# Kernel tuning notes

Measured on AMD Instinct MI355X. Metric: run time of the kernel, lower is better.

The kernel has to match this reference:

```python
import jax, jax.numpy as jnp
import numpy as np

B, C, H, W = 8, 128, 64, 64
U, TOP_K, L, HID = 8, 2, 10, 128


def setup_inputs() -> dict:
    key = jax.random.key(0)
    ks = jax.random.split(key, 16)
    rn = lambda k, shp, s=0.05: jax.random.normal(k, shp, jnp.float32) * s
    return {
        "x": jax.random.normal(ks[0], (B, C, H, W), jnp.float32),
        # router shared MLP (torch Linear: y = x @ W.T + b)
        "W1": rn(ks[1], (HID, C)), "b1": rn(ks[2], (HID,), 0.01),
        "W2": rn(ks[3], (HID, HID)), "b2": rn(ks[4], (HID,), 0.01),
        "W3": rn(ks[5], (HID // 2, HID)), "b3": rn(ks[6], (HID // 2,), 0.01),
        "W4": rn(ks[7], (HID // 2, HID // 2)), "b4": rn(ks[8], (HID // 2,), 0.01),
        "Wu": rn(ks[9], (U, HID // 2)), "bu": rn(ks[10], (U,), 0.01),
        "Wc": rn(ks[11], (L, HID // 2)), "bc": rn(ks[12], (L,), 0.01),
        # per-unit 3x3 convs stacked for a grouped conv: [U*Cout, Cin, 3, 3]
        "conv_w": rn(ks[13], (U * C, C, 3, 3), 0.05),
        "conv_b": rn(ks[14], (U * C,), 0.01),
    }


def reference(x, W1, b1, W2, b2, W3, b3, W4, b4, Wu, bu, Wc, bc, conv_w, conv_b):
    Bt, Ct, Ht, Wt = x.shape
    # --- TopKRouter ---
    pooled = x.mean(axis=(2, 3))                      # adaptive avg pool to 1x1 -> [B,C]
    h = jax.nn.relu(pooled @ W1.T + b1)
    h = jax.nn.relu(h @ W2.T + b2)
    h = jax.nn.relu(h @ W3.T + b3)
    feat = h @ W4.T + b4                              # [B, 64]
    unit_scores = feat @ Wu.T + bu                    # [B, U]
    cls_logits = feat @ Wc.T + bc                     # [B, L]
    noise = jax.random.normal(jax.random.key(42), unit_scores.shape, unit_scores.dtype) * 0.01
    unit_scores = unit_scores + noise
    top_v, top_i = jax.lax.top_k(unit_scores, TOP_K)  # [B, K]
    probabilities = jax.nn.softmax(top_v, axis=1)     # computed in original (unused in combine)
    del probabilities
    unit_usage = jnp.zeros((U,), x.dtype).at[top_i.reshape(-1)].add(1.0) / (Bt * TOP_K)
    lb_loss = ((unit_usage - unit_usage.mean()) ** 2).mean()
    l2_reg = 0.01 * sum(jnp.linalg.norm(p) for p in
                        [W1, b1, W2, b2, W3, b3, W4, b4, Wu, bu, Wc, bc])
    # --- scatter-dispatch: unit u gets x if u in top-k indices else zeros ---
    mask = (top_i[:, :, None] == jnp.arange(U)[None, None, :]).any(axis=1)  # [B, U]
    unit_in = x[:, None] * mask[:, :, None, None, None].astype(x.dtype)     # [B,U,C,H,W]
    # --- per-unit conv as one grouped conv ---
    lhs = unit_in.reshape(Bt, U * Ct, Ht, Wt)
    out = jax.lax.conv_general_dilated(
        lhs, conv_w, window_strides=(1, 1), padding="SAME",
        dimension_numbers=("NCHW", "OIHW", "NCHW"), feature_group_count=U)
    out = out + conv_b[None, :, None, None]
    combined = out.reshape(Bt, U, -1, Ht, Wt)          # [B,U,Cout,H,W]
    # --- gated combine ---
    gate = jax.nn.softmax(combined.mean(axis=(2, 3, 4)), axis=-1)  # [B, U]
    final = jnp.einsum("buchw,bu->bchw", combined, gate)
    return (final, cls_logits, l2_reg, top_i, lb_loss)
```

## Files before the change

### kernel.cpp

```cpp
#include <hip/hip_runtime.h>
#include <math.h>

#define Bn   8
#define Cn   128
#define Hn   64
#define Wn   64
#define HWn  4096
#define Un   8
#define Ln   10
#define HIDn 128

#define OUT_FINAL 0
#define OUT_CLS   4194304
#define OUT_L2    4194384
#define OUT_TOPI  4194385
#define OUT_LB    4194401

#define WS_POOLED 0
#define WS_STR    1024
#define WS_TOPI   10240
#define WS_GSEL   10256
#define WS_BIASC  10272
#define WS_L2P    11296
#define WS_GSUM   11308
#define WS_BSUM   11372
#define WS_H1     11380
#define WS_H2     12404
#define WS_H3     13428
#define WS_FEAT   13940
#define WS_W9P    14452
#define WS_XT     88180
#define WS_WCOMB  2185332

#define NOISE_PARTITIONABLE 1

typedef __attribute__((ext_vector_type(8))) short bf16x8;
typedef __attribute__((ext_vector_type(4))) float f32x4;

__device__ __forceinline__ unsigned short f2bf(float f) {
    unsigned u = __float_as_uint(f);
    unsigned r = (u + 0x7fffu + ((u >> 16) & 1u)) >> 16;
    return (unsigned short)r;
}

__device__ __forceinline__ unsigned rotl32(unsigned x, int d) {
    return (x << d) | (x >> (32 - d));
}

__device__ __forceinline__ void threefry2x32(unsigned k1, unsigned k2,
                                             unsigned c0, unsigned c1,
                                             unsigned* o0, unsigned* o1) {
    unsigned ks0 = k1, ks1 = k2, ks2 = k1 ^ k2 ^ 0x1BD11BDAu;
    unsigned ksa[3] = {ks0, ks1, ks2};
    const int rot[2][4] = {{13, 15, 26, 6}, {17, 29, 16, 24}};
    unsigned x0 = c0 + ks0, x1 = c1 + ks1;
    #pragma unroll
    for (int s = 0; s < 5; ++s) {
        #pragma unroll
        for (int q = 0; q < 4; ++q) {
            x0 += x1;
            x1 = rotl32(x1, rot[s & 1][q]);
            x1 ^= x0;
        }
        x0 += ksa[(s + 1) % 3];
        x1 += ksa[(s + 2) % 3] + (unsigned)(s + 1);
    }
    *o0 = x0;
    *o1 = x1;
}

__device__ float jax_noise_elem(int i) {
    unsigned o0, o1, bits;
#if NOISE_PARTITIONABLE
    threefry2x32(0u, 42u, 0u, (unsigned)i, &o0, &o1);
    bits = o0 ^ o1;
#else
    {
        int second = (i >= 32);
        unsigned j = (unsigned)(second ? i - 32 : i);
        threefry2x32(0u, 42u, j, j + 32u, &o0, &o1);
        bits = second ? o1 : o0;
    }
#endif
    unsigned fb = (bits >> 9) | 0x3f800000u;
    float f = __uint_as_float(fb) - 1.0f;
    const float lo = __uint_as_float(0xBF7FFFFFu);
    float u = f * (1.0f - lo) + lo;
    u = fmaxf(lo, u);
    float w = -log1pf(-u * u);
    float p;
    if (w < 5.0f) {
        w = w - 2.5f;
        p = 2.81022636e-08f;
        p = fmaf(p, w, 3.43273939e-07f);
        p = fmaf(p, w, -3.5233877e-06f);
        p = fmaf(p, w, -4.39150654e-06f);
        p = fmaf(p, w, 0.00021858087f);
        p = fmaf(p, w, -0.00125372503f);
        p = fmaf(p, w, -0.00417768164f);
        p = fmaf(p, w, 0.246640727f);
        p = fmaf(p, w, 1.50140941f);
    } else {
        w = sqrtf(w) - 3.0f;
        p = -0.000200214257f;
        p = fmaf(p, w, 0.000100950558f);
        p = fmaf(p, w, 0.00134934322f);
        p = fmaf(p, w, -0.00367342844f);
        p = fmaf(p, w, 0.00573950773f);
        p = fmaf(p, w, -0.0076224613f);
        p = fmaf(p, w, 0.00943887047f);
        p = fmaf(p, w, 1.00167406f);
        p = fmaf(p, w, 2.83297682f);
    }
    float n = 1.41421356237309515f * (p * u);
    return n * 0.01f;
}

__global__ __launch_bounds__(256) void prep_kernel(
    const float* __restrict__ x, const float* __restrict__ cw,
    const float* __restrict__ W1, const float* __restrict__ b1,
    const float* __restrict__ W2, const float* __restrict__ b2,
    const float* __restrict__ W3, const float* __restrict__ b3,
    const float* __restrict__ W4, const float* __restrict__ b4,
    const float* __restrict__ Wu, const float* __restrict__ bu,
    const float* __restrict__ Wc, const float* __restrict__ bc,
    float* __restrict__ ws) {
    __shared__ float smem[8256];
    int bid = blockIdx.x;
    int tid = threadIdx.x;

    if (bid < 512) {
        int b = bid >> 6, y = bid & 63;
        #pragma unroll
        for (int k = 0; k < 32; ++k) {
            int cin = (tid >> 6) + (k << 2);
            int xcol = tid & 63;
            smem[xcol * 129 + cin] =
                x[(((size_t)b * 128 + cin) << 12) + (y << 6) + xcol];
        }
        __syncthreads();
        unsigned short* xtp = (unsigned short*)(ws + WS_XT);
        #pragma unroll
        for (int i = 0; i < 4; ++i) {
            int op = tid + (i << 8);
            int px = op >> 4, part = op & 15;
            const float* src = smem + px * 129 + part * 8;
            uint4 u;
            u.x = (unsigned)f2bf(src[0]) | ((unsigned)f2bf(src[1]) << 16);
            u.y = (unsigned)f2bf(src[2]) | ((unsigned)f2bf(src[3]) << 16);
            u.z = (unsigned)f2bf(src[4]) | ((unsigned)f2bf(src[5]) << 16);
            u.w = (unsigned)f2bf(src[6]) | ((unsigned)f2bf(src[7]) << 16);
            *(uint4*)(xtp + (((((size_t)b * 64 + y) * 64 + px) << 7) + (part << 3))) = u;
        }
    } else if (bid < 1536) {
        int bc_ = bid - 512;
        const float4* p4 = (const float4*)(x + (size_t)bc_ * HWn);
        float vals[5] = {0.f, 0.f, 0.f, 0.f, 0.f};
        #pragma unroll
        for (int it = 0; it < 4; ++it) {
            int i = tid + it * 256;
            float4 v = p4[i];
            float s4 = v.x + v.y + v.z + v.w;
            vals[0] += s4;
            if (i < 16) vals[1] += s4;
            if (i >= 1008) vals[2] += s4;
            if ((i & 15) == 0) vals[3] += v.x;
            if ((i & 15) == 15) vals[4] += v.w;
            if (i == 0) ws[WS_STR + bc_ * 9 + 5] = v.x;
            if (i == 15) ws[WS_STR + bc_ * 9 + 6] = v.w;
            if (i == 1008) ws[WS_STR + bc_ * 9 + 7] = v.x;
            if (i == 1023) ws[WS_STR + bc_ * 9 + 8] = v.w;
        }
        #pragma unroll
        for (int q = 0; q < 5; ++q)
            #pragma unroll
            for (int off = 32; off > 0; off >>= 1)
                vals[q] += __shfl_xor(vals[q], off);
        int wave = tid >> 6, lane = tid & 63;
        if (lane == 0) {
            #pragma unroll
            for (int q = 0; q < 5; ++q) smem[wave * 5 + q] = vals[q];
        }
        __syncthreads();
        if (tid < 5) {
            float o = smem[tid] + smem[5 + tid] + smem[10 + tid] + smem[15 + tid];
            ws[WS_STR + bc_ * 9 + tid] = o;
            if (tid == 0) ws[WS_POOLED + bc_] = o * (1.0f / HWn);
        }
    } else if (bid < 1600) {
        int idx = bid - 1536;
        int u = idx >> 3, g = idx & 7;
        const float* base = cw + (size_t)u * 147456 + (size_t)g * 18432;
        float a0 = 0.f, a1 = 0.f, a2 = 0.f, a3 = 0.f, a4 = 0.f;
        #pragma unroll
        for (int cout = 0; cout < 16; ++cout) {
            const float* row = base + (size_t)cout * 1152;
            a0 += row[tid];
            a1 += row[tid + 256];
            a2 += row[tid + 512];
            a3 += row[tid + 768];
            if (tid < 128) a4 += row[tid + 1024];
        }
        float* dst = ws + WS_W9P + (size_t)idx * 1152;
        dst[tid] = a0;
        dst[tid + 256] = a1;
        dst[tid + 512] = a2;
        dst[tid + 768] = a3;
        if (tid < 128) dst[tid + 1024] = a4;
    } else {
        int idx = bid - 1600;
        const float* ptab[12] = {W1, b1, W2, b2, W3, b3, W4, b4, Wu, bu, Wc, bc};
        const int ntab[12] = {16384, 128, 16384, 128, 8192, 64, 4096, 64, 512, 8, 640, 10};
        const float* p = ptab[idx];
        int n = ntab[idx];
        float s = 0.f;
        for (int i = tid; i < n; i += 256) { float v = p[i]; s = fmaf(v, v, s); }
        #pragma unroll
        for (int off = 32; off > 0; off >>= 1) s += __shfl_xor(s, off);
        int wave = tid >> 6, lane = tid & 63;
        if (lane == 0) smem[wave] = s;
        __syncthreads();
        if (tid == 0) ws[WS_L2P + idx] = smem[0] + smem[1] + smem[2] + smem[3];
    }
}

__global__ __launch_bounds__(256) void gsum_kernel(const float* __restrict__ cb,
                                                   float* __restrict__ ws) {
    int bid = blockIdx.x;
    int b = bid >> 3, u = bid & 7;
    int tid = threadIdx.x;
    __shared__ float T[1152];
    __shared__ float red[4];

    if (tid < 128) {
        const float* st = ws + WS_STR + (b * 128 + tid) * 9;
        float S = st[0], R0 = st[1], R63 = st[2], C0 = st[3], C63 = st[4];
        float c00 = st[5], c0r = st[6], cb0 = st[7], cbr = st[8];
        float Rex[3] = {R63, 0.f, R0};
        float Cex[3] = {C63, 0.f, C0};
        float crn[3][3] = {{cbr, 0.f, cb0}, {0.f, 0.f, 0.f}, {c0r, 0.f, c00}};
        #pragma unroll
        for (int ky = 0; ky < 3; ++ky)
            #pragma unroll
            for (int kx = 0; kx < 3; ++kx)
                T[tid * 9 + ky * 3 + kx] = S - Rex[ky] - Cex[kx] + crn[ky][kx];
    }
    __syncthreads();

    float s = 0.f;
    #pragma unroll
    for (int g = 0; g < 8; ++g) {
        const float* row = ws + WS_W9P + (size_t)((u << 3) + g) * 1152;
        #pragma unroll
        for (int i = 0; i < 4; ++i)
            s = fmaf(row[tid + i * 256], T[tid + i * 256], s);
        if (tid < 128) s = fmaf(row[tid + 1024], T[tid + 1024], s);
    }
    #pragma unroll
    for (int off = 32; off > 0; off >>= 1) s += __shfl_xor(s, off);
    int wave = tid >> 6, lane = tid & 63;
    if (lane == 0) red[wave] = s;
    __syncthreads();
    if (tid == 0) ws[WS_GSUM + bid] = red[0] + red[1] + red[2] + red[3];

    if (b == 0) {
        float t2 = (tid < 128) ? cb[u * 128 + tid] : 0.f;
        #pragma unroll
        for (int off = 32; off > 0; off >>= 1) t2 += __shfl_xor(t2, off);
        if (lane == 0) red[wave] = t2;
        __syncthreads();
        if (tid == 0) ws[WS_BSUM + u] = red[0] + red[1] + red[2] + red[3];
    }
}

__global__ __launch_bounds__(256) void mlp128_kernel(
    const float* __restrict__ W, const float* __restrict__ bias,
    const float* __restrict__ inp, float* __restrict__ outp,
    int outStride, int doRelu) {
    __shared__ float in_s[1024];
    int tid = threadIdx.x;
    for (int i = tid; i < 1024; i += 256) in_s[i] = inp[i];
    __syncthreads();
    int r = tid >> 5, l = tid & 31;
    int j = blockIdx.x * 8 + r;
    float4 w = ((const float4*)(W + j * 128))[l];
    float bj = bias[j];
    #pragma unroll
    for (int b = 0; b < 8; ++b) {
        const float* sp = in_s + b * 128 + l * 4;
        float s = w.x * sp[0] + w.y * sp[1] + w.z * sp[2] + w.w * sp[3];
        s += __shfl_xor(s, 16, 32); s += __shfl_xor(s, 8, 32);
        s += __shfl_xor(s, 4, 32);  s += __shfl_xor(s, 2, 32);
        s += __shfl_xor(s, 1, 32);
        if (l == 0) {
            s += bj;
            outp[b * outStride + j] = doRelu ? fmaxf(s, 0.f) : s;
        }
    }
}

__global__ __launch_bounds__(256) void mlp64_kernel(
    const float* __restrict__ W, const float* __restrict__ bias,
    const float* __restrict__ inp, float* __restrict__ outp) {
    __shared__ float in_s[512];
    int tid = threadIdx.x;
    for (int i = tid; i < 512; i += 256) in_s[i] = inp[i];
    __syncthreads();
    int r = tid >> 5, l = tid & 31;
    int j = blockIdx.x * 8 + r;
    float2 w = ((const float2*)(W + j * 64))[l];
    float bj = bias[j];
    #pragma unroll
    for (int b = 0; b < 8; ++b) {
        const float* sp = in_s + b * 64 + l * 2;
        float s = w.x * sp[0] + w.y * sp[1];
        s += __shfl_xor(s, 16, 32); s += __shfl_xor(s, 8, 32);
        s += __shfl_xor(s, 4, 32);  s += __shfl_xor(s, 2, 32);
        s += __shfl_xor(s, 1, 32);
        if (l == 0) outp[b * 64 + j] = s + bj;
    }
}

__global__ __launch_bounds__(256) void score_gate_kernel(
    const float* __restrict__ Wu, const float* __restrict__ bu,
    const float* __restrict__ Wc, const float* __restrict__ bc,
    const float* __restrict__ cb,
    float* __restrict__ ws, float* __restrict__ out) {
    __shared__ float feat[512];
    __shared__ float scores[64];
    __shared__ float noise[64];
    __shared__ int topi[16];
    __shared__ float gate_sh[64];
    int tid = threadIdx.x;
    int grp = tid >> 4, l = tid & 15;

    for (int i = tid; i < 512; i += 256) feat[i] = ws[WS_FEAT + i];
    __syncthreads();

    if (tid < 64) noise[tid] = jax_noise_elem(tid);
    if (grp < 8) {
        int j = grp;
        float4 wa = ((const float4*)(Wu + j * 64))[l];
        float bj = bu[j];
        #pragma unroll
        for (int b = 0; b < 8; ++b) {
            const float* sp = feat + b * 64 + l * 4;
            float s = wa.x * sp[0] + wa.y * sp[1] + wa.z * sp[2] + wa.w * sp[3];
            s += __shfl_xor(s, 8, 16); s += __shfl_xor(s, 4, 16);
            s += __shfl_xor(s, 2, 16); s += __shfl_xor(s, 1, 16);
            if (l == 0) scores[b * 8 + j] = s + bj;
        }
    }
    if (grp < 10) {
        int j = grp;
        float4 wa = ((const float4*)(Wc + j * 64))[l];
        float bj = bc[j];
        #pragma unroll
        for (int b = 0; b < 8; ++b) {
            const float* sp = feat + b * 64 + l * 4;
            float s = wa.x * sp[0] + wa.y * sp[1] + wa.z * sp[2] + wa.w * sp[3];
            s += __shfl_xor(s, 8, 16); s += __shfl_xor(s, 4, 16);
            s += __shfl_xor(s, 2, 16); s += __shfl_xor(s, 1, 16);
            if (l == 0) out[OUT_CLS + b * 10 + j] = s + bj;
        }
    }
    __syncthreads();
    if (tid < 64) scores[tid] += noise[tid];
    __syncthreads();
    if (tid < Bn) {
        int b = tid;
        float best = -1e30f; int bi = 0;
        for (int u = 0; u < Un; ++u) {
            float v = scores[b * Un + u];
            if (v > best) { best = v; bi = u; }
        }
        float best2 = -1e30f; int bi2 = 0;
        for (int u = 0; u < Un; ++u) {
            if (u == bi) continue;
            float v = scores[b * Un + u];
            if (v > best2) { best2 = v; bi2 = u; }
        }
        topi[b * 2] = bi;
        topi[b * 2 + 1] = bi2;
        ((int*)ws)[WS_TOPI + b * 2] = bi;
        ((int*)ws)[WS_TOPI + b * 2 + 1] = bi2;
        out[OUT_TOPI + b * 2] = (float)bi;
        out[OUT_TOPI + b * 2 + 1] = (float)bi2;
    }
    __syncthreads();
    if (tid == 0) {
        int cnt[Un];
        for (int u = 0; u < Un; ++u) cnt[u] = 0;
        for (int i = 0; i < Bn * 2; ++i) cnt[topi[i]]++;
        float lb = 0.f;
        for (int u = 0; u < Un; ++u) {
            float d = (float)cnt[u] * (1.f / 16.f) - 0.125f;
            lb += d * d;
        }
        out[OUT_LB] = lb * (1.f / Un);
        float l2 = 0.f;
        #pragma unroll
        for (int i = 0; i < 12; ++i) l2 += sqrtf(ws[WS_L2P + i]);
        out[OUT_L2] = 0.01f * l2;
    }
    if (tid < Bn) {
        int b2 = tid;
        int s0 = topi[b2 * 2], s1 = topi[b2 * 2 + 1];
        float lg[Un];
        for (int u2 = 0; u2 < Un; ++u2) lg[u2] = ws[WS_BSUM + u2] * (1.0f / Cn);
        lg[s0] += ws[WS_GSUM + b2 * 8 + s0] * (1.0f / (Cn * HWn));
        lg[s1] += ws[WS_GSUM + b2 * 8 + s1] * (1.0f / (Cn * HWn));
        float m = -1e30f;
        for (int u2 = 0; u2 < Un; ++u2) m = fmaxf(m, lg[u2]);
        float den = 0.f, e[Un];
        for (int u2 = 0; u2 < Un; ++u2) { e[u2] = expf(lg[u2] - m); den += e[u2]; }
        float inv = 1.0f / den;
        for (int u2 = 0; u2 < Un; ++u2) gate_sh[b2 * Un + u2] = e[u2] * inv;
        ws[WS_GSEL + b2 * 2] = gate_sh[b2 * Un + s0];
        ws[WS_GSEL + b2 * 2 + 1] = gate_sh[b2 * Un + s1];
    }
    __syncthreads();
    for (int i = tid; i < Bn * Cn; i += 256) {
        int b2 = i >> 7, c = i & 127;
        float s = 0.f;
        for (int u2 = 0; u2 < Un; ++u2)
            s = fmaf(gate_sh[b2 * Un + u2], cb[u2 * Cn + c], s);
        ws[WS_BIASC + i] = s;
    }
}

__global__ __launch_bounds__(256) void wprep_kernel(const float* __restrict__ cw,
                                                    float* __restrict__ ws) {
    int bid = blockIdx.x;
    int b = bid >> 5, g = bid & 31;
    const int* topi = (const int*)ws + WS_TOPI;
    int u0 = topi[b * 2], u1 = topi[b * 2 + 1];
    float g0 = ws[WS_GSEL + b * 2], g1 = ws[WS_GSEL + b * 2 + 1];
    __shared__ float lds[1152];
    unsigned short* wc = (unsigned short*)(ws + WS_WCOMB);
    int tid = threadIdx.x;
    for (int co = 0; co < 4; ++co) {
        int cout = g * 4 + co;
        const float* r0 = cw + ((size_t)u0 * 128 + cout) * 1152;
        const float* r1 = cw + ((size_t)u1 * 128 + cout) * 1152;
        if (co) __syncthreads();
        #pragma unroll
        for (int i = 0; i < 5; ++i) {
            int e = tid + i * 256;
            if (e < 1152) lds[e] = g0 * r0[e] + g1 * r1[e];
        }
        __syncthreads();
        #pragma unroll
        for (int i = 0; i < 3; ++i) {
            int p = tid + i * 256;
            if (p < 576) {
                int tap = p >> 6, cp = p & 63;
                unsigned lo = f2bf(lds[(2 * cp) * 9 + tap]);
                unsigned hi = f2bf(lds[(2 * cp + 1) * 9 + tap]);
                *(unsigned*)(wc + ((((size_t)(b * 128 + cout) * 9 + tap) << 7)
                                   + 2 * cp)) = lo | (hi << 16);
            }
        }
    }
}

__global__ __launch_bounds__(128) void conv_mfma_kernel(
    const float* __restrict__ wsf, float* __restrict__ out) {
    const unsigned short* __restrict__ xt = (const unsigned short*)(wsf + WS_XT);
    const unsigned short* __restrict__ wc = (const unsigned short*)(wsf + WS_WCOMB);

    int bid = blockIdx.x;
    int b = bid >> 6, y = bid & 63;
    int tid = threadIdx.x;
    int wave = tid >> 6, lane = tid & 63;
    int quad = lane >> 4, l15 = lane & 15;
    int m0 = wave << 6;

    __shared__ __align__(16) unsigned short xs[198 * 136];

    f32x4 acc[4][4];
    #pragma unroll
    for (int mt = 0; mt < 4; ++mt)
        #pragma unroll
        for (int nt = 0; nt < 4; ++nt)
            acc[mt][nt] = (f32x4){0.f, 0.f, 0.f, 0.f};

    #pragma unroll
    for (int i = 0; i < 25; ++i) {
        int o = tid + i * 128;
        if (o < 3168) {
            int px = o >> 4, part = o & 15;
            int r3 = (unsigned)px / 66u;
            int col = px - r3 * 66;
            int ry = y + r3 - 1;
            int gx = col - 1;
            uint4 v = {0u, 0u, 0u, 0u};
            if ((unsigned)ry < 64u && (unsigned)gx < 64u) {
                v = *(const uint4*)(xt +
                    ((((size_t)b * 64 + ry) * 64 + gx) << 7) + (part << 3));
            }
            *(uint4*)((char*)xs + px * 272 + part * 16) = v;
        }
    }
    __syncthreads();

    int ldsrd = l15 * 272 + quad * 16;
    #pragma unroll
    for (int tap = 0; tap < 9; ++tap) {
        const int dy = tap / 3, dx = tap % 3;
        #pragma unroll
        for (int chunk = 0; chunk < 4; ++chunk) {
            bf16x8 af[4];
            #pragma unroll
            for (int mt = 0; mt < 4; ++mt) {
                int cout = m0 + mt * 16 + l15;
                af[mt] = *(const bf16x8*)(wc +
                    (((size_t)(b * 128 + cout) * 9 + tap) << 7) +
                    (chunk << 5) + (quad << 3));
            }
            bf16x8 bfr[4];
            #pragma unroll
            for (int nt = 0; nt < 4; ++nt) {
                int off = (dy * 66 + dx + nt * 16) * 272 + (chunk << 6);
                bfr[nt] = *(const bf16x8*)((char*)xs + ldsrd + off);
            }
            #pragma unroll
            for (int mt = 0; mt < 4; ++mt)
                #pragma unroll
                for (int nt = 0; nt < 4; ++nt)
                    acc[mt][nt] = __builtin_amdgcn_mfma_f32_16x16x32_bf16(
                        af[mt], bfr[nt], acc[mt][nt], 0, 0, 0);
        }
    }

    #pragma unroll
    for (int mt = 0; mt < 4; ++mt) {
        #pragma unroll
        for (int r = 0; r < 4; ++r) {
            int c = m0 + mt * 16 + (quad << 2) + r;
            float bias = wsf[WS_BIASC + (b << 7) + c];
            size_t rowb = (((size_t)b * 128 + c) << 12) + (y << 6);
            #pragma unroll
            for (int nt = 0; nt < 4; ++nt)
                out[rowb + nt * 16 + l15] = acc[mt][nt][r] + bias;
        }
    }
}

extern "C" void kernel_launch(void* const* d_in, const int* in_sizes, int n_in,
                              void* d_out, int out_size, void* d_ws, size_t ws_size,
                              hipStream_t stream) {
    const float* x  = (const float*)d_in[0];
    const float* W1 = (const float*)d_in[1];
    const float* b1 = (const float*)d_in[2];
    const float* W2 = (const float*)d_in[3];
    const float* b2 = (const float*)d_in[4];
    const float* W3 = (const float*)d_in[5];
    const float* b3 = (const float*)d_in[6];
    const float* W4 = (const float*)d_in[7];
    const float* b4 = (const float*)d_in[8];
    const float* Wu = (const float*)d_in[9];
    const float* bu = (const float*)d_in[10];
    const float* Wc = (const float*)d_in[11];
    const float* bc = (const float*)d_in[12];
    const float* cw = (const float*)d_in[13];
    const float* cb = (const float*)d_in[14];
    float* out = (float*)d_out;
    float* ws  = (float*)d_ws;

    prep_kernel<<<1612, 256, 0, stream>>>(x, cw, W1, b1, W2, b2, W3, b3,
                                          W4, b4, Wu, bu, Wc, bc, ws);
    gsum_kernel<<<64, 256, 0, stream>>>(cb, ws);
    mlp128_kernel<<<16, 256, 0, stream>>>(W1, b1, ws + WS_POOLED, ws + WS_H1, 128, 1);
    mlp128_kernel<<<16, 256, 0, stream>>>(W2, b2, ws + WS_H1, ws + WS_H2, 128, 1);
    mlp128_kernel<<<8, 256, 0, stream>>>(W3, b3, ws + WS_H2, ws + WS_H3, 64, 1);
    mlp64_kernel<<<8, 256, 0, stream>>>(W4, b4, ws + WS_H3, ws + WS_FEAT);
    score_gate_kernel<<<1, 256, 0, stream>>>(Wu, bu, Wc, bc, cb, ws, out);
    wprep_kernel<<<256, 256, 0, stream>>>(cw, ws);
    conv_mfma_kernel<<<512, 128, 0, stream>>>(ws, out);
}
```

Measured before the change: 189.2 us.

## Fuse router MLP, gsum and gating kernels into one grid-barrier kernel

Replaces six small sequential launches (gsum, four MLP layers, score/gate) with one persistent 80-block kernel that uses atomic grid barriers between stages. The gsum work runs alongside the first MLP layer, and the bias-combine step is spread across four blocks. This removes several kernel-launch and drain gaps on the critical path. In exchange it relies on all 80 blocks being co-resident and on a barrier counter that prep_kernel resets, and it adds spin-wait cost at each barrier.

New measurement: 203.9 us. 7.8% more time.

```diff
diff --git a/kernel.cpp b/kernel.cpp
--- a/kernel.cpp
+++ b/kernel.cpp
@@ -28,11 +28,14 @@
 #define WS_H2     12404
 #define WS_H3     13428
 #define WS_FEAT   13940
-#define WS_W9P    14452
-#define WS_XT     88180
-#define WS_WCOMB  2185332
+#define WS_GATE   14452
+#define WS_BAR    14516
+#define WS_W9P    14524
+#define WS_XT     88252
+#define WS_WCOMB  2185404
 
 #define NOISE_PARTITIONABLE 1
+#define RGRID 80u
 
 typedef __attribute__((ext_vector_type(8))) short bf16x8;
 typedef __attribute__((ext_vector_type(4))) float f32x4;
@@ -41,6 +44,17 @@
     unsigned u = __float_as_uint(f);
     unsigned r = (u + 0x7fffu + ((u >> 16) & 1u)) >> 16;
     return (unsigned short)r;
+}
+
+__device__ __forceinline__ void grid_bar(unsigned* bar, int slot) {
+    __syncthreads();
+    if (threadIdx.x == 0) {
+        unsigned* c = bar + slot;
+        __hip_atomic_fetch_add(c, 1u, __ATOMIC_ACQ_REL, __HIP_MEMORY_SCOPE_AGENT);
+        while (__hip_atomic_load(c, __ATOMIC_ACQUIRE, __HIP_MEMORY_SCOPE_AGENT) < RGRID)
+            __builtin_amdgcn_s_sleep(1);
+    }
+    __syncthreads();
 }
 
 __device__ __forceinline__ unsigned rotl32(unsigned x, int d) {
@@ -190,6 +204,7 @@
     } else if (bid < 1600) {
         int idx = bid - 1536;
         int u = idx >> 3, g = idx & 7;
+        if (idx == 0 && tid < 8) ((unsigned*)(ws + WS_BAR))[tid] = 0u;
         const float* base = cw + (size_t)u * 147456 + (size_t)g * 18432;
         float a0 = 0.f, a1 = 0.f, a2 = 0.f, a3 = 0.f, a4 = 0.f;
         #pragma unroll
@@ -224,207 +239,242 @@
     }
 }
 
-__global__ __launch_bounds__(256) void gsum_kernel(const float* __restrict__ cb,
-                                                   float* __restrict__ ws) {
-    int bid = blockIdx.x;
-    int b = bid >> 3, u = bid & 7;
-    int tid = threadIdx.x;
-    __shared__ float T[1152];
-    __shared__ float red[4];
-
-    if (tid < 128) {
-        const float* st = ws + WS_STR + (b * 128 + tid) * 9;
-        float S = st[0], R0 = st[1], R63 = st[2], C0 = st[3], C63 = st[4];
-        float c00 = st[5], c0r = st[6], cb0 = st[7], cbr = st[8];
-        float Rex[3] = {R63, 0.f, R0};
-        float Cex[3] = {C63, 0.f, C0};
-        float crn[3][3] = {{cbr, 0.f, cb0}, {0.f, 0.f, 0.f}, {c0r, 0.f, c00}};
-        #pragma unroll
-        for (int ky = 0; ky < 3; ++ky)
-            #pragma unroll
-            for (int kx = 0; kx < 3; ++kx)
-                T[tid * 9 + ky * 3 + kx] = S - Rex[ky] - Cex[kx] + crn[ky][kx];
-    }
-    __syncthreads();
-
-    float s = 0.f;
-    #pragma unroll
-    for (int g = 0; g < 8; ++g) {
-        const float* row = ws + WS_W9P + (size_t)((u << 3) + g) * 1152;
-        #pragma unroll
-        for (int i = 0; i < 4; ++i)
-            s = fmaf(row[tid + i * 256], T[tid + i * 256], s);
-        if (tid < 128) s = fmaf(row[tid + 1024], T[tid + 1024], s);
-    }
-    #pragma unroll
-    for (int off = 32; off > 0; off >>= 1) s += __shfl_xor(s, off);
-    int wave = tid >> 6, lane = tid & 63;
-    if (lane == 0) red[wave] = s;
-    __syncthreads();
-    if (tid == 0) ws[WS_GSUM + bid] = red[0] + red[1] + red[2] + red[3];
-
-    if (b == 0) {
-        float t2 = (tid < 128) ? cb[u * 128 + tid] : 0.f;
-        #pragma unroll
-        for (int off = 32; off > 0; off >>= 1) t2 += __shfl_xor(t2, off);
-        if (lane == 0) red[wave] = t2;
-        __syncthreads();
-        if (tid == 0) ws[WS_BSUM + u] = red[0] + red[1] + red[2] + red[3];
-    }
-}
-
-__global__ __launch_bounds__(256) void mlp128_kernel(
-    const float* __restrict__ W, const float* __restrict__ bias,
-    const float* __restrict__ inp, float* __restrict__ outp,
-    int outStride, int doRelu) {
-    __shared__ float in_s[1024];
-    int tid = threadIdx.x;
-    for (int i = tid; i < 1024; i += 256) in_s[i] = inp[i];
-    __syncthreads();
-    int r = tid >> 5, l = tid & 31;
-    int j = blockIdx.x * 8 + r;
-    float4 w = ((const float4*)(W + j * 128))[l];
-    float bj = bias[j];
-    #pragma unroll
-    for (int b = 0; b < 8; ++b) {
-        const float* sp = in_s + b * 128 + l * 4;
-        float s = w.x * sp[0] + w.y * sp[1] + w.z * sp[2] + w.w * sp[3];
-        s += __shfl_xor(s, 16, 32); s += __shfl_xor(s, 8, 32);
-        s += __shfl_xor(s, 4, 32);  s += __shfl_xor(s, 2, 32);
-        s += __shfl_xor(s, 1, 32);
-        if (l == 0) {
-            s += bj;
-            outp[b * outStride + j] = doRelu ? fmaxf(s, 0.f) : s;
-        }
-    }
-}
-
-__global__ __launch_bounds__(256) void mlp64_kernel(
-    const float* __restrict__ W, const float* __restrict__ bias,
-    const float* __restrict__ inp, float* __restrict__ outp) {
-    __shared__ float in_s[512];
-    int tid = threadIdx.x;
-    for (int i = tid; i < 512; i += 256) in_s[i] = inp[i];
-    __syncthreads();
-    int r = tid >> 5, l = tid & 31;
-    int j = blockIdx.x * 8 + r;
-    float2 w = ((const float2*)(W + j * 64))[l];
-    float bj = bias[j];
-    #pragma unroll
-    for (int b = 0; b < 8; ++b) {
-        const float* sp = in_s + b * 64 + l * 2;
-        float s = w.x * sp[0] + w.y * sp[1];
-        s += __shfl_xor(s, 16, 32); s += __shfl_xor(s, 8, 32);
-        s += __shfl_xor(s, 4, 32);  s += __shfl_xor(s, 2, 32);
-        s += __shfl_xor(s, 1, 32);
-        if (l == 0) outp[b * 64 + j] = s + bj;
-    }
-}
-
-__global__ __launch_bounds__(256) void score_gate_kernel(
+__global__ __launch_bounds__(256) void router_fused_kernel(
+    const float* __restrict__ W1, const float* __restrict__ b1,
+    const float* __restrict__ W2, const float* __restrict__ b2,
+    const float* __restrict__ W3, const float* __restrict__ b3,
+    const float* __restrict__ W4, const float* __restrict__ b4,
     const float* __restrict__ Wu, const float* __restrict__ bu,
     const float* __restrict__ Wc, const float* __restrict__ bc,
     const float* __restrict__ cb,
     float* __restrict__ ws, float* __restrict__ out) {
-    __shared__ float feat[512];
-    __shared__ float scores[64];
-    __shared__ float noise[64];
-    __shared__ int topi[16];
-    __shared__ float gate_sh[64];
+    __shared__ float sh[1216];
+    int bid = blockIdx.x;
     int tid = threadIdx.x;
-    int grp = tid >> 4, l = tid & 15;
-
-    for (int i = tid; i < 512; i += 256) feat[i] = ws[WS_FEAT + i];
-    __syncthreads();
-
-    if (tid < 64) noise[tid] = jax_noise_elem(tid);
-    if (grp < 8) {
-        int j = grp;
-        float4 wa = ((const float4*)(Wu + j * 64))[l];
-        float bj = bu[j];
+    unsigned* bar = (unsigned*)(ws + WS_BAR);
+
+    if (bid < 16) {
+        for (int i = tid; i < 1024; i += 256) sh[i] = ws[WS_POOLED + i];
+        __syncthreads();
+        int r = tid >> 5, l = tid & 31;
+        int j = bid * 8 + r;
+        float4 w = ((const float4*)(W1 + j * 128))[l];
+        float bj = b1[j];
         #pragma unroll
         for (int b = 0; b < 8; ++b) {
-            const float* sp = feat + b * 64 + l * 4;
-            float s = wa.x * sp[0] + wa.y * sp[1] + wa.z * sp[2] + wa.w * sp[3];
-            s += __shfl_xor(s, 8, 16); s += __shfl_xor(s, 4, 16);
-            s += __shfl_xor(s, 2, 16); s += __shfl_xor(s, 1, 16);
-            if (l == 0) scores[b * 8 + j] = s + bj;
-        }
-    }
-    if (grp < 10) {
-        int j = grp;
-        float4 wa = ((const float4*)(Wc + j * 64))[l];
-        float bj = bc[j];
+            const float* sp = sh + b * 128 + l * 4;
+            float s = w.x * sp[0] + w.y * sp[1] + w.z * sp[2] + w.w * sp[3];
+            s += __shfl_xor(s, 16, 32); s += __shfl_xor(s, 8, 32);
+            s += __shfl_xor(s, 4, 32);  s += __shfl_xor(s, 2, 32);
+            s += __shfl_xor(s, 1, 32);
+            if (l == 0) ws[WS_H1 + b * 128 + j] = fmaxf(s + bj, 0.f);
+        }
+    } else {
+        int idx = bid - 16;
+        int b = idx >> 3, u = idx & 7;
+        float* T = sh;
+        float* red = sh + 1152;
+        if (tid < 128) {
+            const float* st = ws + WS_STR + (b * 128 + tid) * 9;
+            float S = st[0], R0 = st[1], R63 = st[2], C0 = st[3], C63 = st[4];
+            float c00 = st[5], c0r = st[6], cb0 = st[7], cbr = st[8];
+            float Rex[3] = {R63, 0.f, R0};
+            float Cex[3] = {C63, 0.f, C0};
+            float crn[3][3] = {{cbr, 0.f, cb0}, {0.f, 0.f, 0.f}, {c0r, 0.f, c00}};
+            #pragma unroll
+            for (int ky = 0; ky < 3; ++ky)
+                #pragma unroll
+                for (int kx = 0; kx < 3; ++kx)
+                    T[tid * 9 + ky * 3 + kx] = S - Rex[ky] - Cex[kx] + crn[ky][kx];
+        }
+        __syncthreads();
+        float s = 0.f;
+        #pragma unroll
+        for (int g = 0; g < 8; ++g) {
+            const float* row = ws + WS_W9P + (size_t)((u << 3) + g) * 1152;
+            #pragma unroll
+            for (int i = 0; i < 4; ++i)
+                s = fmaf(row[tid + i * 256], T[tid + i * 256], s);
+            if (tid < 128) s = fmaf(row[tid + 1024], T[tid + 1024], s);
+        }
+        #pragma unroll
+        for (int off = 32; off > 0; off >>= 1) s += __shfl_xor(s, off);
+        int wave = tid >> 6, lane = tid & 63;
+        if (lane == 0) red[wave] = s;
+        __syncthreads();
+        if (tid == 0) ws[WS_GSUM + idx] = red[0] + red[1] + red[2] + red[3];
+        if (b == 0) {
+            float t2 = (tid < 128) ? cb[u * 128 + tid] : 0.f;
+            #pragma unroll
+            for (int off = 32; off > 0; off >>= 1) t2 += __shfl_xor(t2, off);
+            if (lane == 0) red[wave] = t2;
+            __syncthreads();
+            if (tid == 0) ws[WS_BSUM + u] = red[0] + red[1] + red[2] + red[3];
+        }
+    }
+    grid_bar(bar, 0);
+
+    if (bid < 16) {
+        for (int i = tid; i < 1024; i += 256) sh[i] = ws[WS_H1 + i];
+        __syncthreads();
+        int r = tid >> 5, l = tid & 31;
+        int j = bid * 8 + r;
+        float4 w = ((const float4*)(W2 + j * 128))[l];
+        float bj = b2[j];
         #pragma unroll
         for (int b = 0; b < 8; ++b) {
-            const float* sp = feat + b * 64 + l * 4;
-            float s = wa.x * sp[0] + wa.y * sp[1] + wa.z * sp[2] + wa.w * sp[3];
-            s += __shfl_xor(s, 8, 16); s += __shfl_xor(s, 4, 16);
-            s += __shfl_xor(s, 2, 16); s += __shfl_xor(s, 1, 16);
-            if (l == 0) out[OUT_CLS + b * 10 + j] = s + bj;
-        }
-    }
-    __syncthreads();
-    if (tid < 64) scores[tid] += noise[tid];
-    __syncthreads();
-    if (tid < Bn) {
-        int b = tid;
-        float best = -1e30f; int bi = 0;
-        for (int u = 0; u < Un; ++u) {
-            float v = scores[b * Un + u];
-            if (v > best) { best = v; bi = u; }
-        }
-        float best2 = -1e30f; int bi2 = 0;
-        for (int u = 0; u < Un; ++u) {
-            if (u == bi) continue;
-            float v = scores[b * Un + u];
-            if (v > best2) { best2 = v; bi2 = u; }
-        }
-        topi[b * 2] = bi;
-        topi[b * 2 + 1] = bi2;
-        ((int*)ws)[WS_TOPI + b * 2] = bi;
-        ((int*)ws)[WS_TOPI + b * 2 + 1] = bi2;
-        out[OUT_TOPI + b * 2] = (float)bi;
-        out[OUT_TOPI + b * 2 + 1] = (float)bi2;
-    }
-    __syncthreads();
-    if (tid == 0) {
-        int cnt[Un];
-        for (int u = 0; u < Un; ++u) cnt[u] = 0;
-        for (int i = 0; i < Bn * 2; ++i) cnt[topi[i]]++;
-        float lb = 0.f;
-        for (int u = 0; u < Un; ++u) {
-            float d = (float)cnt[u] * (1.f / 16.f) - 0.125f;
-            lb += d * d;
-        }
-        out[OUT_LB] = lb * (1.f / Un);
-        float l2 = 0.f;
-        #pragma unroll
-        for (int i = 0; i < 12; ++i) l2 += sqrtf(ws[WS_L2P + i]);
-        out[OUT_L2] = 0.01f * l2;
-    }
-    if (tid < Bn) {
-        int b2 = tid;
-        int s0 = topi[b2 * 2], s1 = topi[b2 * 2 + 1];
-        float lg[Un];
-        for (int u2 = 0; u2 < Un; ++u2) lg[u2] = ws[WS_BSUM + u2] * (1.0f / Cn);
-        lg[s0] += ws[WS_GSUM + b2 * 8 + s0] * (1.0f / (Cn * HWn));
-        lg[s1] += ws[WS_GSUM + b2 * 8 + s1] * (1.0f / (Cn * HWn));
-        float m = -1e30f;
-        for (int u2 = 0; u2 < Un; ++u2) m = fmaxf(m, lg[u2]);
-        float den = 0.f, e[Un];
-        for (int u2 = 0; u2 < Un; ++u2) { e[u2] = expf(lg[u2] - m); den += e[u2]; }
-        float inv = 1.0f / den;
-        for (int u2 = 0; u2 < Un; ++u2) gate_sh[b2 * Un + u2] = e[u2] * inv;
-        ws[WS_GSEL + b2 * 2] = gate_sh[b2 * Un + s0];
-        ws[WS_GSEL + b2 * 2 + 1] = gate_sh[b2 * Un + s1];
-    }
-    __syncthreads();
-    for (int i = tid; i < Bn * Cn; i += 256) {
+            const float* sp = sh + b * 128 + l * 4;
+            float s = w.x * sp[0] + w.y * sp[1] + w.z * sp[2] + w.w * sp[3];
+            s += __shfl_xor(s, 16, 32); s += __shfl_xor(s, 8, 32);
+            s += __shfl_xor(s, 4, 32);  s += __shfl_xor(s, 2, 32);
+            s += __shfl_xor(s, 1, 32);
+            if (l == 0) ws[WS_H2 + b * 128 + j] = fmaxf(s + bj, 0.f);
+        }
+    }
+    grid_bar(bar, 1);
+
+    if (bid < 8) {
+        for (int i = tid; i < 1024; i += 256) sh[i] = ws[WS_H2 + i];
+        __syncthreads();
+        int r = tid >> 5, l = tid & 31;
+        int j = bid * 8 + r;
+        float4 w = ((const float4*)(W3 + j * 128))[l];
+        float bj = b3[j];
+        #pragma unroll
+        for (int b = 0; b < 8; ++b) {
+            const float* sp = sh + b * 128 + l * 4;
+            float s = w.x * sp[0] + w.y * sp[1] + w.z * sp[2] + w.w * sp[3];
+            s += __shfl_xor(s, 16, 32); s += __shfl_xor(s, 8, 32);
+            s += __shfl_xor(s, 4, 32);  s += __shfl_xor(s, 2, 32);
+            s += __shfl_xor(s, 1, 32);
+            if (l == 0) ws[WS_H3 + b * 64 + j] = fmaxf(s + bj, 0.f);
+        }
+    }
+    grid_bar(bar, 2);
+
+    if (bid < 8) {
+        for (int i = tid; i < 512; i += 256) sh[i] = ws[WS_H3 + i];
+        __syncthreads();
+        int r = tid >> 5, l = tid & 31;
+        int j = bid * 8 + r;
+        float2 w = ((const float2*)(W4 + j * 64))[l];
+        float bj = b4[j];
+        #pragma unroll
+        for (int b = 0; b < 8; ++b) {
+            const float* sp = sh + b * 64 + l * 2;
+            float s = w.x * sp[0] + w.y * sp[1];
+            s += __shfl_xor(s, 16, 32); s += __shfl_xor(s, 8, 32);
+            s += __shfl_xor(s, 4, 32);  s += __shfl_xor(s, 2, 32);
+            s += __shfl_xor(s, 1, 32);
+            if (l == 0) ws[WS_FEAT + b * 64 + j] = s + bj;
+        }
+    }
+    grid_bar(bar, 3);
+
+    if (bid == 0) {
+        float* feat = sh;
+        float* scores = sh + 512;
+        float* noise = sh + 576;
+        float* gate = sh + 640;
+        int* topi = (int*)(sh + 704);
+        int grp = tid >> 4, l = tid & 15;
+        for (int i = tid; i < 512; i += 256) feat[i] = ws[WS_FEAT + i];
+        __syncthreads();
+        if (tid < 64) noise[tid] = jax_noise_elem(tid);
+        if (grp < 8) {
+            int j = grp;
+            float4 wa = ((const float4*)(Wu + j * 64))[l];
+            float bj = bu[j];
+            #pragma unroll
+            for (int b = 0; b < 8; ++b) {
+                const float* sp = feat + b * 64 + l * 4;
+                float s = wa.x * sp[0] + wa.y * sp[1] + wa.z * sp[2] + wa.w * sp[3];
+                s += __shfl_xor(s, 8, 16); s += __shfl_xor(s, 4, 16);
+                s += __shfl_xor(s, 2, 16); s += __shfl_xor(s, 1, 16);
+                if (l == 0) scores[b * 8 + j] = s + bj;
+            }
+        }
+        if (grp < 10) {
+            int j = grp;
+            float4 wa = ((const float4*)(Wc + j * 64))[l];
+            float bj = bc[j];
+            #pragma unroll
+            for (int b = 0; b < 8; ++b) {
+                const float* sp = feat + b * 64 + l * 4;
+                float s = wa.x * sp[0] + wa.y * sp[1] + wa.z * sp[2] + wa.w * sp[3];
+                s += __shfl_xor(s, 8, 16); s += __shfl_xor(s, 4, 16);
+                s += __shfl_xor(s, 2, 16); s += __shfl_xor(s, 1, 16);
+                if (l == 0) out[OUT_CLS + b * 10 + j] = s + bj;
+            }
+        }
+        __syncthreads();
+        if (tid < 64) scores[tid] += noise[tid];
+        __syncthreads();
+        if (tid < Bn) {
+            int b = tid;
+            float best = -1e30f; int bi = 0;
+            for (int u = 0; u < Un; ++u) {
+                float v = scores[b * Un + u];
+                if (v > best) { best = v; bi = u; }
+            }
+            float best2 = -1e30f; int bi2 = 0;
+            for (int u = 0; u < Un; ++u) {
+                if (u == bi) continue;
+                float v = scores[b * Un + u];
+                if (v > best2) { best2 = v; bi2 = u; }
+            }
+            topi[b * 2] = bi;
+            topi[b * 2 + 1] = bi2;
+            ((int*)ws)[WS_TOPI + b * 2] = bi;
+            ((int*)ws)[WS_TOPI + b * 2 + 1] = bi2;
+            out[OUT_TOPI + b * 2] = (float)bi;
+            out[OUT_TOPI + b * 2 + 1] = (float)bi2;
+        }
+        __syncthreads();
+        if (tid == 0) {
+            int cnt[Un];
+            for (int u = 0; u < Un; ++u) cnt[u] = 0;
+            for (int i = 0; i < Bn * 2; ++i) cnt[topi[i]]++;
+            float lb = 0.f;
+            for (int u = 0; u < Un; ++u) {
+                float d = (float)cnt[u] * (1.f / 16.f) - 0.125f;
+                lb += d * d;
+            }
+            out[OUT_LB] = lb * (1.f / Un);
+            float l2 = 0.f;
+            #pragma unroll
+            for (int i = 0; i < 12; ++i) l2 += sqrtf(ws[WS_L2P + i]);
+            out[OUT_L2] = 0.01f * l2;
+        }
+        if (tid < Bn) {
+            int b2 = tid;
+            int s0 = topi[b2 * 2], s1 = topi[b2 * 2 + 1];
+            float lg[Un];
+            for (int u2 = 0; u2 < Un; ++u2) lg[u2] = ws[WS_BSUM + u2] * (1.0f / Cn);
+            lg[s0] += ws[WS_GSUM + b2 * 8 + s0] * (1.0f / (Cn * HWn));
+            lg[s1] += ws[WS_GSUM + b2 * 8 + s1] * (1.0f / (Cn * HWn));
+            float m = -1e30f;
+            for (int u2 = 0; u2 < Un; ++u2) m = fmaxf(m, lg[u2]);
+            float den = 0.f, e[Un];
+            for (int u2 = 0; u2 < Un; ++u2) { e[u2] = expf(lg[u2] - m); den += e[u2]; }
+            float inv = 1.0f / den;
+            for (int u2 = 0; u2 < Un; ++u2) {
+                gate[b2 * Un + u2] = e[u2] * inv;
+                ws[WS_GATE + b2 * Un + u2] = e[u2] * inv;
+            }
+            ws[WS_GSEL + b2 * 2] = gate[b2 * Un + s0];
+            ws[WS_GSEL + b2 * 2 + 1] = gate[b2 * Un + s1];
+        }
+    }
+    grid_bar(bar, 4);
+
+    if (bid < 4) {
+        int i = bid * 256 + tid;
         int b2 = i >> 7, c = i & 127;
         float s = 0.f;
+        #pragma unroll
         for (int u2 = 0; u2 < Un; ++u2)
-            s = fmaf(gate_sh[b2 * Un + u2], cb[u2 * Cn + c], s);
+            s = fmaf(ws[WS_GATE + b2 * Un + u2], cb[u2 * Cn + c], s);
         ws[WS_BIASC + i] = s;
     }
 }
@@ -570,12 +620,9 @@
 
     prep_kernel<<<1612, 256, 0, stream>>>(x, cw, W1, b1, W2, b2, W3, b3,
                                           W4, b4, Wu, bu, Wc, bc, ws);
-    gsum_kernel<<<64, 256, 0, stream>>>(cb, ws);
-    mlp128_kernel<<<16, 256, 0, stream>>>(W1, b1, ws + WS_POOLED, ws + WS_H1, 128, 1);
-    mlp128_kernel<<<16, 256, 0, stream>>>(W2, b2, ws + WS_H1, ws + WS_H2, 128, 1);
-    mlp128_kernel<<<8, 256, 0, stream>>>(W3, b3, ws + WS_H2, ws + WS_H3, 64, 1);
-    mlp64_kernel<<<8, 256, 0, stream>>>(W4, b4, ws + WS_H3, ws + WS_FEAT);
-    score_gate_kernel<<<1, 256, 0, stream>>>(Wu, bu, Wc, bc, cb, ws, out);
+    router_fused_kernel<<<RGRID, 256, 0, stream>>>(W1, b1, W2, b2, W3, b3,
+                                                   W4, b4, Wu, bu, Wc, bc,
+                                                   cb, ws, out);
     wprep_kernel<<<256, 256, 0, stream>>>(cw, ws);
     conv_mfma_kernel<<<512, 128, 0, stream>>>(ws, out);
 }
```
